# Kernel optimization log

Hardware: AMD Instinct MI355X
Metric: run time of the kernel (lower is better)

Reference implementation:

```python
import jax, jax.numpy as jnp
import numpy as np


def setup_inputs() -> dict:
    key = jax.random.key(0)
    k1, k2 = jax.random.split(key)
    latent = jax.random.normal(k1, (131072, 128), dtype=jnp.float32)
    coords = jax.random.normal(k2, (2048, 128), dtype=jnp.float32)
    return {"latent": latent, "coords": coords}


def reference(latent, coords):
    # torch.cdist(latent, coords).min(1)[1]
    # argmin over euclidean distance == argmin over squared distance,
    # so we skip the sqrt (same result, cheaper and numerically safer).
    x2 = jnp.sum(latent * latent, axis=1, keepdims=True)          # [N, 1]
    c2 = jnp.sum(coords * coords, axis=1)                          # [C]
    cross = latent @ coords.T                                      # [N, C]
    d2 = x2 + c2[None, :] - 2.0 * cross                            # [N, C] squared dists
    return jnp.argmin(d2, axis=1)                                  # [N] int indices
```

## Files before the change

kernel.cpp:

```cpp
#include <hip/hip_runtime.h>


constexpr int D = 128;
constexpr int C = 2048;
constexpr int NCH = 64;
constexpr int NCHUNKS = C / NCH;
constexpr float MARGIN = 0.02f;
constexpr int WL_CAP = 32768;

constexpr size_t WS_CNT = 8192;
constexpr size_t WS_WL  = 16384;
constexpr size_t WS_BH  = 262144;
constexpr size_t WS_BL  = 786432;

typedef __attribute__((ext_vector_type(8))) short short8;
typedef __attribute__((ext_vector_type(4))) float f32x4;

__device__ inline unsigned short bf16_rne(float x) {
    unsigned u = __float_as_uint(x);
    u += 0x7FFFu + ((u >> 16) & 1u);
    return (unsigned short)(u >> 16);
}
__device__ inline float bf16_to_f(unsigned short h) {
    return __uint_as_float(((unsigned)h) << 16);
}
__device__ inline void split8(const float* v, short8* hi, short8* lo) {
#pragma unroll
    for (int j = 0; j < 8; ++j) {
        unsigned short h = bf16_rne(v[j]);
        (*hi)[j] = (short)h;
        (*lo)[j] = (short)bf16_rne(v[j] - bf16_to_f(h));
    }
}

__global__ void prep_coords(const float* __restrict__ coords,
                            unsigned short* __restrict__ Bh,
                            unsigned short* __restrict__ Bl,
                            float* __restrict__ c2, int* __restrict__ counter) {
    int t = blockIdx.x * blockDim.x + threadIdx.x;
    if (t == 0) *counter = 0;
    if (t >= C * 16) return;
    int c  = t >> 4;
    int k8 = t & 15;
    float v[8];
    *(float4*)(v)     = *(const float4*)(coords + (size_t)c * D + k8 * 8);
    *(float4*)(v + 4) = *(const float4*)(coords + (size_t)c * D + k8 * 8 + 4);
    short8 hi, lo;
    split8(v, &hi, &lo);
    int ch = c >> 6, nl = c & 63;
    size_t off = (size_t)ch * (NCH * 128) + ((size_t)nl * 16 + (k8 ^ (nl & 15))) * 8;
    *(short8*)(Bh + off) = hi;
    *(short8*)(Bl + off) = lo;
    float p = 0.f;
#pragma unroll
    for (int j = 0; j < 8; ++j) p = fmaf(v[j], v[j], p);
#pragma unroll
    for (int m = 1; m <= 8; m <<= 1) p += __shfl_xor(p, m, 64);
    if (k8 == 0) c2[c] = p;
}


__global__ __launch_bounds__(256, 3) void centroid_fast(
        const float* __restrict__ latent,
        const unsigned short* __restrict__ Bh_img,
        const unsigned short* __restrict__ Bl_img,
        const float* __restrict__ c2g,
        int* __restrict__ out,
        int* __restrict__ counter,
        int* __restrict__ worklist) {
    __shared__ __align__(16) unsigned short Bh[NCH * 128], Bl[NCH * 128];
    __shared__ float sc2[NCH];

    const int tid  = threadIdx.x;
    const int wid  = tid >> 6;
    const int lane = tid & 63;
    const int q    = lane >> 4, lr = lane & 15;
    const int row_block = blockIdx.x * 128;

    short8 Ah[2][4], Al[2][4];
#pragma unroll
    for (int mt = 0; mt < 2; ++mt) {
        const float* rp = latent + (size_t)(row_block + wid * 32 + mt * 16 + lr) * D;
#pragma unroll
        for (int ks = 0; ks < 4; ++ks) {
            float v[8];
            *(float4*)(v)     = *(const float4*)(rp + ks * 32 + q * 8);
            *(float4*)(v + 4) = *(const float4*)(rp + ks * 32 + q * 8 + 4);
            split8(v, &Ah[mt][ks], &Al[mt][ks]);
        }
    }

    float b1[8], b2[8];
    int   bidx[8];
#pragma unroll
    for (int s = 0; s < 8; ++s) { b1[s] = 3.4e38f; b2[s] = 3.4e38f; bidx[s] = 0; }

    for (int ch = 0; ch < NCHUNKS; ++ch) {
        __syncthreads();
        {
            const unsigned short* sh = Bh_img + (size_t)ch * (NCH * 128);
            const unsigned short* sl = Bl_img + (size_t)ch * (NCH * 128);
#pragma unroll
            for (int i = 0; i < 4; ++i) {
                int e = (i * 256 + tid) * 8;
                *(short8*)(Bh + e) = *(const short8*)(sh + e);
                *(short8*)(Bl + e) = *(const short8*)(sl + e);
            }
            if (tid < NCH) sc2[tid] = c2g[ch * NCH + tid];
        }
        __syncthreads();

#pragma unroll
        for (int nt = 0; nt < 4; ++nt) {
            const int nl = nt * 16 + lr;
            f32x4 acc[2];
#pragma unroll
            for (int mt = 0; mt < 2; ++mt) acc[mt] = (f32x4){0.f, 0.f, 0.f, 0.f};
#pragma unroll
            for (int ks = 0; ks < 4; ++ks) {
                const int xv = ((ks * 4) | q) ^ lr;
                const int e  = nl * 128 + xv * 8;
                short8 bh = *(const short8*)(Bh + e);
                short8 bl = *(const short8*)(Bl + e);
#pragma unroll
                for (int mt = 0; mt < 2; ++mt) {
                    acc[mt] = __builtin_amdgcn_mfma_f32_16x16x32_bf16(Ah[mt][ks], bh, acc[mt], 0, 0, 0);
                    acc[mt] = __builtin_amdgcn_mfma_f32_16x16x32_bf16(Ah[mt][ks], bl, acc[mt], 0, 0, 0);
                    acc[mt] = __builtin_amdgcn_mfma_f32_16x16x32_bf16(Al[mt][ks], bh, acc[mt], 0, 0, 0);
                }
            }
            const float c2v = sc2[nl];
            const int n_global = ch * NCH + nl;
#pragma unroll
            for (int mt = 0; mt < 2; ++mt)
#pragma unroll
                for (int r = 0; r < 4; ++r) {
                    int slot = mt * 4 + r;
                    float s = fmaf(-2.f, acc[mt][r], c2v);
                    bool lt = s < b1[slot];
                    float t = fmaxf(s, b1[slot]);
                    b2[slot]   = fminf(b2[slot], t);
                    b1[slot]   = fminf(s, b1[slot]);
                    bidx[slot] = lt ? n_global : bidx[slot];
                }
        }
    }

#pragma unroll
    for (int m = 1; m <= 8; m <<= 1) {
#pragma unroll
        for (int s = 0; s < 8; ++s) {
            float ob1 = __shfl_xor(b1[s], m, 64);
            float ob2 = __shfl_xor(b2[s], m, 64);
            int   oix = __shfl_xor(bidx[s], m, 64);
            float mx  = fmaxf(b1[s], ob1);
            b2[s] = fminf(fminf(b2[s], ob2), mx);
            bool take = (ob1 < b1[s]) || (ob1 == b1[s] && oix < bidx[s]);
            b1[s]   = take ? ob1 : b1[s];
            bidx[s] = take ? oix : bidx[s];
        }
    }
#pragma unroll
    for (int s = 0; s < 8; ++s) {
        if (lr == s) {
            int row = row_block + wid * 32 + (s >> 2) * 16 + q * 4 + (s & 3);
            out[row] = bidx[s];
            if (b2[s] - b1[s] < MARGIN) {
                int w = atomicAdd(counter, 1);
                if (w < WL_CAP) worklist[w] = row;
            }
        }
    }
}


__global__ __launch_bounds__(256) void refine_fp64(
        const float* __restrict__ latent, const float* __restrict__ coords,
        const int* __restrict__ worklist, const int* __restrict__ counter,
        int wl_cap, int* __restrict__ out) {
    __shared__ float  xs[D];
    __shared__ double rv[256];
    __shared__ int    ri[256];

    int n = *counter;
    if (n > wl_cap) n = wl_cap;

    for (int wi = blockIdx.x; wi < n; wi += gridDim.x) {
        int row = worklist[wi];
        if (threadIdx.x < D)
            xs[threadIdx.x] = latent[(size_t)row * D + threadIdx.x];
        __syncthreads();

        double best = 1.0e300;
        int    bix  = 0;
        for (int c = threadIdx.x; c < C; c += 256) {
            const float4* cp = (const float4*)(coords + (size_t)c * D);
            double s = 0.0;
#pragma unroll 8
            for (int k4 = 0; k4 < 32; ++k4) {
                float4 v = cp[k4];
                double d0 = (double)xs[k4 * 4 + 0] - (double)v.x;
                double d1 = (double)xs[k4 * 4 + 1] - (double)v.y;
                double d2 = (double)xs[k4 * 4 + 2] - (double)v.z;
                double d3 = (double)xs[k4 * 4 + 3] - (double)v.w;
                s = fma(d0, d0, s); s = fma(d1, d1, s);
                s = fma(d2, d2, s); s = fma(d3, d3, s);
            }
            if (s < best) { best = s; bix = c; }
        }
        rv[threadIdx.x] = best;
        ri[threadIdx.x] = bix;
        __syncthreads();
        for (int off = 128; off > 0; off >>= 1) {
            if (threadIdx.x < off) {
                double ov = rv[threadIdx.x + off];
                int    oi = ri[threadIdx.x + off];
                if (ov < rv[threadIdx.x] ||
                    (ov == rv[threadIdx.x] && oi < ri[threadIdx.x])) {
                    rv[threadIdx.x] = ov;
                    ri[threadIdx.x] = oi;
                }
            }
            __syncthreads();
        }
        if (threadIdx.x == 0) out[row] = ri[0];
        __syncthreads();
    }
}

extern "C" void kernel_launch(void* const* d_in, const int* in_sizes, int n_in,
                              void* d_out, int out_size, void* d_ws, size_t ws_size,
                              hipStream_t stream) {
    const float* latent = (const float*)d_in[0];
    const float* coords = (const float*)d_in[1];
    int*         out    = (int*)d_out;

    char* ws = (char*)d_ws;
    float* c2      = (float*)ws;
    int*   counter = (int*)(ws + WS_CNT);
    int*   wl      = (int*)(ws + WS_WL);
    unsigned short* Bh = (unsigned short*)(ws + WS_BH);
    unsigned short* Bl = (unsigned short*)(ws + WS_BL);
    const int n_rows = in_sizes[0] / D;

    prep_coords<<<(C * 16) / 256, 256, 0, stream>>>(coords, Bh, Bl, c2, counter);
    centroid_fast<<<n_rows / 128, 256, 0, stream>>>(latent, Bh, Bl, c2, out,
                                                    counter, wl);
    refine_fp64<<<608, 256, 0, stream>>>(latent, coords, wl, counter, WL_CAP, out);
}
```

Baseline: 333.2 us.

## Double-buffer coord chunks via async LDS loads and widen row tile per wave

Streams coordinate chunks into LDS with global_load_lds into a double buffer, prefetching the next chunk while the current one feeds MFMAs, and loads all c2 norms once. Each wave now handles 64 rows instead of 32, doubling B-tile reuse, and -0.5*c2 is folded into the accumulator init so the epilogue becomes a max-tracking compare. The refine kernel splits its fp64 sum into four accumulators to break the dependency chain. Register pressure rises and occupancy drops to two blocks per CU; the margin is halved to match the rescaled score, so the set of rows sent to refinement stays about the same.

```diff
diff --git a/kernel.cpp b/kernel.cpp
--- a/kernel.cpp
+++ b/kernel.cpp
@@ -5,7 +5,7 @@
 constexpr int C = 2048;
 constexpr int NCH = 64;
 constexpr int NCHUNKS = C / NCH;
-constexpr float MARGIN = 0.02f;
+constexpr float MARGIN_H = 0.01f;
 constexpr int WL_CAP = 32768;
 
 constexpr size_t WS_CNT = 8192;
@@ -15,6 +15,7 @@
 
 typedef __attribute__((ext_vector_type(8))) short short8;
 typedef __attribute__((ext_vector_type(4))) float f32x4;
+typedef unsigned int u32;
 
 __device__ inline unsigned short bf16_rne(float x) {
     unsigned u = __float_as_uint(x);
@@ -31,6 +32,12 @@
         (*hi)[j] = (short)h;
         (*lo)[j] = (short)bf16_rne(v[j] - bf16_to_f(h));
     }
+}
+
+__device__ __forceinline__ void gl_lds16(const void* g, void* l) {
+    __builtin_amdgcn_global_load_lds(
+        (const __attribute__((address_space(1))) u32*)g,
+        (__attribute__((address_space(3))) u32*)l, 16, 0, 0);
 }
 
 __global__ void prep_coords(const float* __restrict__ coords,
@@ -60,7 +67,7 @@
 }
 
 
-__global__ __launch_bounds__(256, 3) void centroid_fast(
+__global__ __launch_bounds__(256, 2) void centroid_fast(
         const float* __restrict__ latent,
         const unsigned short* __restrict__ Bh_img,
         const unsigned short* __restrict__ Bl_img,
@@ -68,19 +75,35 @@
         int* __restrict__ out,
         int* __restrict__ counter,
         int* __restrict__ worklist) {
-    __shared__ __align__(16) unsigned short Bh[NCH * 128], Bl[NCH * 128];
-    __shared__ float sc2[NCH];
+    __shared__ __align__(16) unsigned short Bh[2][NCH * 128], Bl[2][NCH * 128];
+    __shared__ __align__(16) float sc2[C];
 
     const int tid  = threadIdx.x;
     const int wid  = tid >> 6;
     const int lane = tid & 63;
     const int q    = lane >> 4, lr = lane & 15;
-    const int row_block = blockIdx.x * 128;
-
-    short8 Ah[2][4], Al[2][4];
-#pragma unroll
-    for (int mt = 0; mt < 2; ++mt) {
-        const float* rp = latent + (size_t)(row_block + wid * 32 + mt * 16 + lr) * D;
+    const int row_block = blockIdx.x * 256;
+
+    {
+        const unsigned short* sh = Bh_img;
+        const unsigned short* sl = Bl_img;
+#pragma unroll
+        for (int i = 0; i < 4; ++i) {
+            int e = (i * 256 + tid) * 8;
+            gl_lds16(sh + e, &Bh[0][e]);
+            gl_lds16(sl + e, &Bl[0][e]);
+        }
+    }
+#pragma unroll
+    for (int i = 0; i < 2; ++i) {
+        int e = (i * 256 + tid) * 4;
+        *(float4*)(sc2 + e) = *(const float4*)(c2g + e);
+    }
+
+    short8 Ah[4][4], Al[4][4];
+#pragma unroll
+    for (int mt = 0; mt < 4; ++mt) {
+        const float* rp = latent + (size_t)(row_block + wid * 64 + mt * 16 + lr) * D;
 #pragma unroll
         for (int ks = 0; ks < 4; ++ks) {
             float v[8];
@@ -90,82 +113,90 @@
         }
     }
 
-    float b1[8], b2[8];
-    int   bidx[8];
-#pragma unroll
-    for (int s = 0; s < 8; ++s) { b1[s] = 3.4e38f; b2[s] = 3.4e38f; bidx[s] = 0; }
+    float b1[16], b2[16];
+    int   bidx[16];
+#pragma unroll
+    for (int s = 0; s < 16; ++s) { b1[s] = -3.4e38f; b2[s] = -3.4e38f; bidx[s] = 0; }
+
+    __syncthreads();
 
     for (int ch = 0; ch < NCHUNKS; ++ch) {
-        __syncthreads();
-        {
-            const unsigned short* sh = Bh_img + (size_t)ch * (NCH * 128);
-            const unsigned short* sl = Bl_img + (size_t)ch * (NCH * 128);
+        const int buf = ch & 1;
+        if (ch + 1 < NCHUNKS) {
+            const unsigned short* sh = Bh_img + (size_t)(ch + 1) * (NCH * 128);
+            const unsigned short* sl = Bl_img + (size_t)(ch + 1) * (NCH * 128);
 #pragma unroll
             for (int i = 0; i < 4; ++i) {
                 int e = (i * 256 + tid) * 8;
-                *(short8*)(Bh + e) = *(const short8*)(sh + e);
-                *(short8*)(Bl + e) = *(const short8*)(sl + e);
-            }
-            if (tid < NCH) sc2[tid] = c2g[ch * NCH + tid];
-        }
-        __syncthreads();
+                gl_lds16(sh + e, &Bh[buf ^ 1][e]);
+                gl_lds16(sl + e, &Bl[buf ^ 1][e]);
+            }
+            asm volatile("s_waitcnt vmcnt(8)" ::: "memory");
+        } else {
+            asm volatile("s_waitcnt vmcnt(0)" ::: "memory");
+        }
+        __builtin_amdgcn_s_barrier();
 
 #pragma unroll
         for (int nt = 0; nt < 4; ++nt) {
             const int nl = nt * 16 + lr;
-            f32x4 acc[2];
-#pragma unroll
-            for (int mt = 0; mt < 2; ++mt) acc[mt] = (f32x4){0.f, 0.f, 0.f, 0.f};
+            const float mh = -0.5f * sc2[ch * NCH + nl];
+            f32x4 acc[4];
+#pragma unroll
+            for (int mt = 0; mt < 4; ++mt) acc[mt] = (f32x4){mh, mh, mh, mh};
 #pragma unroll
             for (int ks = 0; ks < 4; ++ks) {
                 const int xv = ((ks * 4) | q) ^ lr;
                 const int e  = nl * 128 + xv * 8;
-                short8 bh = *(const short8*)(Bh + e);
-                short8 bl = *(const short8*)(Bl + e);
-#pragma unroll
-                for (int mt = 0; mt < 2; ++mt) {
+                short8 bh = *(const short8*)(&Bh[buf][e]);
+                short8 bl = *(const short8*)(&Bl[buf][e]);
+#pragma unroll
+                for (int mt = 0; mt < 4; ++mt)
                     acc[mt] = __builtin_amdgcn_mfma_f32_16x16x32_bf16(Ah[mt][ks], bh, acc[mt], 0, 0, 0);
+#pragma unroll
+                for (int mt = 0; mt < 4; ++mt)
                     acc[mt] = __builtin_amdgcn_mfma_f32_16x16x32_bf16(Ah[mt][ks], bl, acc[mt], 0, 0, 0);
+#pragma unroll
+                for (int mt = 0; mt < 4; ++mt)
                     acc[mt] = __builtin_amdgcn_mfma_f32_16x16x32_bf16(Al[mt][ks], bh, acc[mt], 0, 0, 0);
-                }
-            }
-            const float c2v = sc2[nl];
+            }
             const int n_global = ch * NCH + nl;
 #pragma unroll
-            for (int mt = 0; mt < 2; ++mt)
+            for (int mt = 0; mt < 4; ++mt)
 #pragma unroll
                 for (int r = 0; r < 4; ++r) {
                     int slot = mt * 4 + r;
-                    float s = fmaf(-2.f, acc[mt][r], c2v);
-                    bool lt = s < b1[slot];
-                    float t = fmaxf(s, b1[slot]);
-                    b2[slot]   = fminf(b2[slot], t);
-                    b1[slot]   = fminf(s, b1[slot]);
-                    bidx[slot] = lt ? n_global : bidx[slot];
+                    float a = acc[mt][r];
+                    bool gt  = a > b1[slot];
+                    float mn = fminf(a, b1[slot]);
+                    b2[slot]   = fmaxf(b2[slot], mn);
+                    b1[slot]   = fmaxf(a, b1[slot]);
+                    bidx[slot] = gt ? n_global : bidx[slot];
                 }
         }
+        __builtin_amdgcn_s_barrier();
     }
 
 #pragma unroll
     for (int m = 1; m <= 8; m <<= 1) {
 #pragma unroll
-        for (int s = 0; s < 8; ++s) {
-            float ob1 = __shfl_xor(b1[s], m, 64);
-            float ob2 = __shfl_xor(b2[s], m, 64);
-            int   oix = __shfl_xor(bidx[s], m, 64);
-            float mx  = fmaxf(b1[s], ob1);
-            b2[s] = fminf(fminf(b2[s], ob2), mx);
-            bool take = (ob1 < b1[s]) || (ob1 == b1[s] && oix < bidx[s]);
-            b1[s]   = take ? ob1 : b1[s];
-            bidx[s] = take ? oix : bidx[s];
-        }
-    }
-#pragma unroll
-    for (int s = 0; s < 8; ++s) {
+        for (int s = 0; s < 16; ++s) {
+            float oa = __shfl_xor(b1[s], m, 64);
+            float ob = __shfl_xor(b2[s], m, 64);
+            int   oi = __shfl_xor(bidx[s], m, 64);
+            float mn = fminf(b1[s], oa);
+            b2[s] = fmaxf(fmaxf(b2[s], ob), mn);
+            bool take = (oa > b1[s]) || (oa == b1[s] && oi < bidx[s]);
+            b1[s]   = take ? oa : b1[s];
+            bidx[s] = take ? oi : bidx[s];
+        }
+    }
+#pragma unroll
+    for (int s = 0; s < 16; ++s) {
         if (lr == s) {
-            int row = row_block + wid * 32 + (s >> 2) * 16 + q * 4 + (s & 3);
+            int row = row_block + wid * 64 + (s >> 2) * 16 + q * 4 + (s & 3);
             out[row] = bidx[s];
-            if (b2[s] - b1[s] < MARGIN) {
+            if (b1[s] - b2[s] < MARGIN_H) {
                 int w = atomicAdd(counter, 1);
                 if (w < WL_CAP) worklist[w] = row;
             }
@@ -195,7 +226,7 @@
         int    bix  = 0;
         for (int c = threadIdx.x; c < C; c += 256) {
             const float4* cp = (const float4*)(coords + (size_t)c * D);
-            double s = 0.0;
+            double s0 = 0.0, s1 = 0.0, s2 = 0.0, s3 = 0.0;
 #pragma unroll 8
             for (int k4 = 0; k4 < 32; ++k4) {
                 float4 v = cp[k4];
@@ -203,9 +234,10 @@
                 double d1 = (double)xs[k4 * 4 + 1] - (double)v.y;
                 double d2 = (double)xs[k4 * 4 + 2] - (double)v.z;
                 double d3 = (double)xs[k4 * 4 + 3] - (double)v.w;
-                s = fma(d0, d0, s); s = fma(d1, d1, s);
-                s = fma(d2, d2, s); s = fma(d3, d3, s);
-            }
+                s0 = fma(d0, d0, s0); s1 = fma(d1, d1, s1);
+                s2 = fma(d2, d2, s2); s3 = fma(d3, d3, s3);
+            }
+            double s = (s0 + s1) + (s2 + s3);
             if (s < best) { best = s; bix = c; }
         }
         rv[threadIdx.x] = best;
@@ -244,7 +276,7 @@
     const int n_rows = in_sizes[0] / D;
 
     prep_coords<<<(C * 16) / 256, 256, 0, stream>>>(coords, Bh, Bl, c2, counter);
-    centroid_fast<<<n_rows / 128, 256, 0, stream>>>(latent, Bh, Bl, c2, out,
+    centroid_fast<<<n_rows / 256, 256, 0, stream>>>(latent, Bh, Bl, c2, out,
                                                     counter, wl);
     refine_fp64<<<608, 256, 0, stream>>>(latent, coords, wl, counter, WL_CAP, out);
 }
```

Measured after the change: 310.6 us. 1.07x faster.
